# Optimization experiments

Hardware: AMD Instinct MI355X
Metric: run time of the kernel (lower is better)

## Reference

```python
import jax, jax.numpy as jnp
import numpy as np
from jax.scipy.special import logsumexp

UNK_ID = 1
B, T, V = 128, 33, 25000
E, H, D = 256, 256, 512
N, C = 8192, 16384
L = T - 1


def setup_inputs() -> dict:
    key = jax.random.key(0)
    ks = jax.random.split(key, 12)
    input_memories = jax.random.normal(ks[0], (N, D), jnp.float32)
    # each target owns a contiguous block of N//B memories (every segment non-empty)
    origin = jnp.repeat(jnp.arange(B, dtype=jnp.int32), N // B)
    initial_states = jax.random.normal(ks[1], (B, H), jnp.float32)
    target_token_ids = jax.random.randint(ks[2], (B, T), 0, V)
    # copyable elements: pick (memory n, time l); flat idx into [N,L] and [B,L]
    mem_pick = jax.random.randint(ks[3], (C,), 0, N)
    t_pick = jax.random.randint(ks[4], (C,), 0, L)
    copyable_elements_idxs = mem_pick * L + t_pick
    copyable_elements_sample_idxs = origin[mem_pick] * L + t_pick
    target_lengths = jax.random.randint(ks[5], (B,), 1, L + 1)
    emb_weight = 0.02 * jax.random.normal(ks[6], (V, E), jnp.float32)
    gru_w_ih = 0.05 * jax.random.normal(ks[7], (3 * H, E), jnp.float32)
    gru_w_hh = 0.05 * jax.random.normal(ks[8], (3 * H, H), jnp.float32)
    gru_b_ih = jnp.zeros((3 * H,), jnp.float32)
    gru_b_hh = jnp.zeros((3 * H,), jnp.float32)
    w_std_att = 0.05 * jax.random.normal(ks[9], (H, D), jnp.float32)
    w_copy_att = 0.05 * jax.random.normal(ks[10], (H, D), jnp.float32)
    hidden_to_vocab = 0.01 * jax.random.normal(ks[11], (2 * H, E), jnp.float32)
    vocab_bias = jnp.zeros((V,), jnp.float32)
    return dict(input_memories=input_memories, input_memories_origin_idx=origin,
                initial_states=initial_states, target_token_ids=target_token_ids,
                copyable_elements_idxs=copyable_elements_idxs,
                copyable_elements_sample_idxs=copyable_elements_sample_idxs,
                target_lengths=target_lengths, emb_weight=emb_weight,
                gru_w_ih=gru_w_ih, gru_w_hh=gru_w_hh, gru_b_ih=gru_b_ih,
                gru_b_hh=gru_b_hh, w_std_att=w_std_att, w_copy_att=w_copy_att,
                hidden_to_vocab=hidden_to_vocab, vocab_bias=vocab_bias)


def _gru(x, h0, w_ih, w_hh, b_ih, b_hh):
    # x: [B,L,E], h0: [B,H] -> outputs [B,L,H], last state [B,H]
    def step(h, xt):
        gi = xt @ w_ih.T + b_ih
        gh = h @ w_hh.T + b_hh
        ir, iz, inew = jnp.split(gi, 3, axis=-1)
        hr, hz, hnew = jnp.split(gh, 3, axis=-1)
        r = jax.nn.sigmoid(ir + hr)
        z = jax.nn.sigmoid(iz + hz)
        n = jnp.tanh(inew + r * hnew)
        h_next = (1.0 - z) * n + z * h
        return h_next, h_next
    h_last, ys = jax.lax.scan(step, h0, jnp.swapaxes(x, 0, 1))
    return jnp.swapaxes(ys, 0, 1), h_last


def _seg_log_softmax(x, idx, num_seg):
    m = jax.ops.segment_max(x, idx, num_segments=num_seg)
    x_sh = x - m[idx]
    s = jax.ops.segment_sum(jnp.exp(x_sh), idx, num_segments=num_seg)
    return x_sh - jnp.log(s)[idx]


def _seg_logsumexp(x, idx, num_seg):
    m = jax.ops.segment_max(x, idx, num_segments=num_seg)
    m_safe = jnp.where(jnp.isfinite(m), m, 0.0)
    s = jax.ops.segment_sum(jnp.exp(x - m_safe[idx]), idx, num_segments=num_seg)
    return jnp.where(s > 0, jnp.log(jnp.where(s > 0, s, 1.0)) + m_safe, -jnp.inf)


def reference(input_memories, input_memories_origin_idx, initial_states,
              target_token_ids, copyable_elements_idxs,
              copyable_elements_sample_idxs, target_lengths, emb_weight,
              gru_w_ih, gru_w_hh, gru_b_ih, gru_b_hh, w_std_att, w_copy_att,
              hidden_to_vocab, vocab_bias):
    origin = input_memories_origin_idx
    b, t = target_token_ids.shape
    l = t - 1
    tok_in = target_token_ids[:, :-1]
    tok_out = target_token_ids[:, 1:]

    x = emb_weight[tok_in]                                   # [B,L,E]
    out_states, _ = _gru(x, initial_states, gru_w_ih, gru_w_hh, gru_b_ih, gru_b_hh)
    std_reps = input_memories @ w_std_att.T                  # [N,H]
    copy_reps = input_memories @ w_copy_att.T                # [N,H]
    out_per_input = out_states[origin]                       # [N,L,H]
    std_scores = jnp.einsum('nlh,nh->nl', out_per_input, std_reps)
    copy_scores = jnp.einsum('nlh,nh->nl', out_per_input, copy_reps)

    std_logprobs = _seg_log_softmax(std_scores, origin, b)   # [N,L]
    std_mul = jnp.exp(std_logprobs)[:, :, None] * std_reps[:, None, :]
    std_out = jax.ops.segment_sum(std_mul, origin, num_segments=b)  # [B,L,H]

    cat = jnp.concatenate([std_out, out_states], axis=-1)    # [B,L,2H]
    target_scores = (cat @ hidden_to_vocab) @ emb_weight.T + vocab_bias  # [B,L,V]

    total_copy = _seg_logsumexp(copy_scores, origin, b)      # [B,L]
    all_scores = jnp.concatenate([target_scores, total_copy[:, :, None]], axis=-1)
    norm = logsumexp(all_scores, axis=-1)                    # [B,L]
    target_logprobs = target_scores - norm[:, :, None]
    copy_logprobs = copy_scores - norm[origin]               # [N,L]

    num_valid = jax.ops.segment_sum(jnp.ones_like(copyable_elements_sample_idxs),
                                    copyable_elements_sample_idxs,
                                    num_segments=b * l)
    valid_copy = num_valid.reshape(b, l) > 0
    unk_loc = tok_out == UNK_ID
    mask = valid_copy & unk_loc

    gen_lp = jnp.take_along_axis(target_logprobs, tok_out[:, :, None], axis=-1)[..., 0]
    gen_lp = jnp.where(mask, -jnp.inf, gen_lp)

    cc = _seg_logsumexp(copy_logprobs.reshape(-1)[copyable_elements_idxs],
                        copyable_elements_sample_idxs, b * l).reshape(b, l)

    any_lp = logsumexp(jnp.stack([gen_lp, cc]), axis=0)      # [B,L]
    len_mask = (jnp.arange(l)[None, :] < target_lengths[:, None]).astype(jnp.float32)
    per_seq = (any_lp * len_mask).sum(-1) / len_mask.sum(-1)
    return -per_seq.mean()
```

## Files before the change

### kernel.cpp

```cpp
#include <hip/hip_runtime.h>
#include <hip/hip_bf16.h>

#define UNK 1
constexpr int B  = 128, T = 33, V = 25000, E = 256, H = 256, D = 512;
constexpr int N  = 8192, C = 16384, L = 32;
constexpr int BL = B * L;
constexpr int VP = 25088;

typedef __attribute__((ext_vector_type(8))) short bf16x8;
typedef __attribute__((ext_vector_type(4))) float fx4;
typedef unsigned short u16;
typedef unsigned int u32;

__device__ __forceinline__ u16 f2b(float f) {
  u32 u = __float_as_uint(f);
  u += 0x7FFFu + ((u >> 16) & 1u);
  return (u16)(u >> 16);
}
__device__ __forceinline__ float b2f(u16 s) { return __uint_as_float(((u32)s) << 16); }
__device__ __forceinline__ float fsigm(float x) { return 1.f / (1.f + __expf(-x)); }
__device__ __forceinline__ float ftanh(float x) {
  float cx = fminf(fmaxf(x, -15.f), 15.f);
  float e = __expf(2.f * cx);
  return (e - 1.f) / (e + 1.f);
}
__device__ __forceinline__ u32 fkey(float f) {
  u32 b = __float_as_uint(f);
  return (b & 0x80000000u) ? ~b : (b | 0x80000000u);
}
__device__ __forceinline__ float fdec(u32 k) {
  u32 b = (k & 0x80000000u) ? (k & 0x7FFFFFFFu) : ~k;
  return __uint_as_float(b);
}
__device__ __forceinline__ void lcomb(float& M, float& S, float m2, float s2) {
  float Mn = fmaxf(M, m2);
  float a = (S  > 0.f) ? S  * expf(M  - Mn) : 0.f;
  float b = (s2 > 0.f) ? s2 * expf(m2 - Mn) : 0.f;
  M = Mn; S = a + b;
}
__device__ __forceinline__ void gload16(const void* g, void* l) {
  __builtin_amdgcn_global_load_lds(
      (const __attribute__((address_space(1))) void*)g,
      (__attribute__((address_space(3))) void*)l, 16, 0, 0);
}

__device__ __forceinline__ void cvt4_at(const float* in, u16* out, int i) {
  float4 v = *(const float4*)&in[i];
  u16 r[4] = { f2b(v.x), f2b(v.y), f2b(v.z), f2b(v.w) };
  *(ushort4*)&out[i] = *(ushort4*)r;
}

constexpr int EB_GI   = 192;
constexpr int P2_EMB  = VP * E / 1024;
constexpr int P2_MEM  = N * D / 1024;
constexpr int P2_WHH  = 192;
constexpr int P2_WS   = 128;
constexpr int P2_WC   = 128;
constexpr int P2_TR   = 512;
constexpr int P2_INIT = 16;
constexpr int EB2_TOT = EB_GI + P2_EMB + P2_MEM + P2_WHH + P2_WS + P2_WC + P2_TR + P2_INIT;

__global__ __launch_bounds__(256, 2) void k_embgiB2(const int* __restrict__ tok,
    const float* __restrict__ emb, const float* __restrict__ wih,
    const float* __restrict__ bih, const float* __restrict__ bhh,
    float* __restrict__ Git,
    const float* __restrict__ mem, const float* __restrict__ whh,
    const float* __restrict__ wstd, const float* __restrict__ wcpy,
    const float* __restrict__ h2v,
    u16* __restrict__ embb, u16* __restrict__ memb, u16* __restrict__ whb,
    u16* __restrict__ wsb, u16* __restrict__ wcb, u16* __restrict__ h2vtb,
    u32* __restrict__ segk, float* __restrict__ segs,
    int* __restrict__ nval, float* __restrict__ lacc) {
  __shared__ __align__(16) u16 As[2][128 * 64];
  __shared__ __align__(16) u16 Bs2[2][128 * 64];
  int e = blockIdx.x, t = threadIdx.x;
  if (e >= EB_GI) {
    int b = e - EB_GI;
    if (b < P2_EMB) {
      int i = (b * 256 + t) * 4;
      if (i + 3 < V * E) cvt4_at(emb, embb, i);
      else for (int j = 0; j < 4; ++j) embb[i + j] = (i + j < V * E) ? f2b(emb[i + j]) : (u16)0;
      return;
    }
    b -= P2_EMB;
    if (b < P2_MEM) { cvt4_at(mem, memb, (b * 256 + t) * 4); return; }
    b -= P2_MEM;
    if (b < P2_WHH) { cvt4_at(whh, whb, (b * 256 + t) * 4); return; }
    b -= P2_WHH;
    if (b < P2_WS)  { cvt4_at(wstd, wsb, (b * 256 + t) * 4); return; }
    b -= P2_WS;
    if (b < P2_WC)  { cvt4_at(wcpy, wcb, (b * 256 + t) * 4); return; }
    b -= P2_WC;
    if (b < P2_TR) {
      int f = b * 256 + t, j = f >> 9, k = f & 511;
      h2vtb[f] = f2b(h2v[k * 256 + j]);
      return;
    }
    b -= P2_TR;
    int i = b * 256 + t;
    if (i < BL) { segk[i] = 0x007FFFFFu; segs[i] = 0.f; nval[i] = 0; }
    if (i == 0) lacc[0] = 0.f;
    return;
  }
  int m0 = (e & 31) * 128, n0 = (e >> 5) * 128;
  int lane = t & 63, w = t >> 6, wm = w >> 1, wn = w & 1;
  int r16 = lane & 15, hi = lane >> 4;
  char* AsB = (char*)&As[0][0];
  char* BsB = (char*)&Bs2[0][0];
  int tk4[4];
#pragma unroll
  for (int i = 0; i < 4; ++i) {
    int row = (w * 4 + i) * 8 + (lane >> 3);
    int bl = m0 + row;
    tk4[i] = tok[(bl >> 5) * 33 + (bl & 31)];
  }
  fx4 acc[4][4] = {};
  auto stage = [&](int kt, int buf) {
#pragma unroll
    for (int i = 0; i < 4; ++i) {
      int row = (w * 4 + i) * 8 + (lane >> 3);
      int c = (lane & 7) ^ (row & 7);
      float4 a0 = *(const float4*)&emb[tk4[i] * 256 + kt * 64 + c * 8];
      float4 a1 = *(const float4*)&emb[tk4[i] * 256 + kt * 64 + c * 8 + 4];
      __align__(16) u16 ra[8] = { f2b(a0.x), f2b(a0.y), f2b(a0.z), f2b(a0.w),
                                  f2b(a1.x), f2b(a1.y), f2b(a1.z), f2b(a1.w) };
      *(int4*)(AsB + buf * 16384 + (w * 4 + i) * 1024 + lane * 16) = *(const int4*)ra;
      float4 b0 = *(const float4*)&wih[(n0 + row) * 256 + kt * 64 + c * 8];
      float4 b1 = *(const float4*)&wih[(n0 + row) * 256 + kt * 64 + c * 8 + 4];
      __align__(16) u16 rb[8] = { f2b(b0.x), f2b(b0.y), f2b(b0.z), f2b(b0.w),
                                  f2b(b1.x), f2b(b1.y), f2b(b1.z), f2b(b1.w) };
      *(int4*)(BsB + buf * 16384 + (w * 4 + i) * 1024 + lane * 16) = *(const int4*)rb;
    }
  };
  stage(0, 0);
  __syncthreads();
  for (int kt = 0; kt < 4; ++kt) {
    int buf = kt & 1;
    bf16x8 afr[4][2], bfr[4][2];
#pragma unroll
    for (int mi = 0; mi < 4; ++mi)
#pragma unroll
      for (int kk = 0; kk < 2; ++kk) {
        int row = wm * 64 + mi * 16 + r16, cc = kk * 4 + hi;
        afr[mi][kk] = *(const bf16x8*)(AsB + buf * 16384 + (row * 8 + (cc ^ (row & 7))) * 16);
      }
#pragma unroll
    for (int ni = 0; ni < 4; ++ni)
#pragma unroll
      for (int kk = 0; kk < 2; ++kk) {
        int row = wn * 64 + ni * 16 + r16, cc = kk * 4 + hi;
        bfr[ni][kk] = *(const bf16x8*)(BsB + buf * 16384 + (row * 8 + (cc ^ (row & 7))) * 16);
      }
    if (kt < 3) {
      stage(kt + 1, (kt + 1) & 1);
    }
#pragma unroll
    for (int kk = 0; kk < 2; ++kk)
#pragma unroll
      for (int mi = 0; mi < 4; ++mi)
#pragma unroll
        for (int ni = 0; ni < 4; ++ni)
          acc[mi][ni] = __builtin_amdgcn_mfma_f32_16x16x32_bf16(afr[mi][kk], bfr[ni][kk], acc[mi][ni], 0, 0, 0);
    __syncthreads();
  }
  float bihv[4];
#pragma unroll
  for (int ni = 0; ni < 4; ++ni) {
    int j = n0 + wn * 64 + ni * 16 + r16;
    bihv[ni] = bih[j] + (j < 512 ? bhh[j] : 0.f);
  }
#pragma unroll
  for (int mi = 0; mi < 4; ++mi)
#pragma unroll
    for (int ni = 0; ni < 4; ++ni)
#pragma unroll
      for (int q = 0; q < 4; ++q) {
        int bl = m0 + wm * 64 + mi * 16 + hi * 4 + q;
        int b = bl >> 5, st = bl & 31;
        int j  = n0 + wn * 64 + ni * 16 + r16;
        Git[(((size_t)(b >> 4) * 32 + st) * 768 + j) * 16 + (b & 15)] = acc[mi][ni][q] + bihv[ni];
      }
}

__global__ __launch_bounds__(512, 2) void k_grureps(
    const float* __restrict__ Git, const u16* __restrict__ whb,
    const float* __restrict__ bhh, const float* __restrict__ h0,
    u16* __restrict__ outsb,
    const u16* __restrict__ Am, const u16* __restrict__ wsb,
    const u16* __restrict__ wcb, float* __restrict__ sr, float* __restrict__ cr) {
  __shared__ __align__(16) char smem[147456];
  const int t = threadIdx.x;
  const int w = t >> 6, l = t & 63;

  if (blockIdx.x < 8) {
    u16* nfr = (u16*)smem;
    u16* hbf0 = (u16*)(smem + 131072);
    u16* hbf1 = (u16*)(smem + 131072 + 8192);
    const int lj = l & 15, lk = l >> 4;
    const int b0 = blockIdx.x * 16;

    bf16x8 fr[2][8], fz[2][8];
#pragma unroll
    for (int jh = 0; jh < 2; ++jh)
#pragma unroll
      for (int kc = 0; kc < 8; ++kc) {
        int jr = w * 32 + jh * 16 + lj;
        int k0 = kc * 32 + lk * 8;
        fr[jh][kc] = *(const bf16x8*)&whb[(0 * 256 + jr) * 256 + k0];
        fz[jh][kc] = *(const bf16x8*)&whb[(1 * 256 + jr) * 256 + k0];
        int4 nv = *(const int4*)&whb[(2 * 256 + jr) * 256 + k0];
        *(int4*)&nfr[((w * 16 + jh * 8 + kc) * 64 + l) * 8] = nv;
      }
    float bN[2];
#pragma unroll
    for (int jh = 0; jh < 2; ++jh) bN[jh] = bhh[512 + w * 32 + jh * 16 + lj];
    float hst[2][4];
#pragma unroll
    for (int jh = 0; jh < 2; ++jh)
#pragma unroll
      for (int q = 0; q < 4; ++q) {
        int m = lk * 4 + q, j = w * 32 + jh * 16 + lj;
        hst[jh][q] = h0[(b0 + m) * 256 + j];
        hbf0[m * 256 + (((j >> 3) ^ (m & 7)) * 8) + (j & 7)] = f2b(hst[jh][q]);
      }
    __syncthreads();

    for (int st = 0; st < 32; ++st) {
      const float* gb = Git + (size_t)(blockIdx.x * 32 + st) * 768 * 16;
      fx4 grz[4];
#pragma unroll
      for (int g = 0; g < 2; ++g)
#pragma unroll
        for (int jh = 0; jh < 2; ++jh)
          grz[g * 2 + jh] = *(const fx4*)&gb[(g * 256 + w * 32 + jh * 16 + lj) * 16 + lk * 4];
      fx4 gn[2];
      fx4 accR[2] = {}, accZ[2] = {}, accN[2] = {};
      const u16* hb = (st & 1) ? hbf1 : hbf0;
#pragma unroll
      for (int kc = 0; kc < 8; ++kc) {
        int k8 = kc * 4 + lk;
        bf16x8 a = *(const bf16x8*)&hb[lj * 256 + ((k8 ^ (lj & 7)) * 8)];
        bf16x8 nf0 = *(const bf16x8*)&nfr[((w * 16 + 0 + kc) * 64 + l) * 8];
        bf16x8 nf1 = *(const bf16x8*)&nfr[((w * 16 + 8 + kc) * 64 + l) * 8];
        accR[0] = __builtin_amdgcn_mfma_f32_16x16x32_bf16(a, fr[0][kc], accR[0], 0, 0, 0);
        accR[1] = __builtin_amdgcn_mfma_f32_16x16x32_bf16(a, fr[1][kc], accR[1], 0, 0, 0);
        accZ[0] = __builtin_amdgcn_mfma_f32_16x16x32_bf16(a, fz[0][kc], accZ[0], 0, 0, 0);
        accZ[1] = __builtin_amdgcn_mfma_f32_16x16x32_bf16(a, fz[1][kc], accZ[1], 0, 0, 0);
        accN[0] = __builtin_amdgcn_mfma_f32_16x16x32_bf16(a, nf0, accN[0], 0, 0, 0);
        accN[1] = __builtin_amdgcn_mfma_f32_16x16x32_bf16(a, nf1, accN[1], 0, 0, 0);
        if (kc == 5) {
#pragma unroll
          for (int jh = 0; jh < 2; ++jh)
            gn[jh] = *(const fx4*)&gb[(2 * 256 + w * 32 + jh * 16 + lj) * 16 + lk * 4];
        }
      }
      u16* hw = (st & 1) ? hbf0 : hbf1;
#pragma unroll
      for (int jh = 0; jh < 2; ++jh)
#pragma unroll
        for (int q = 0; q < 4; ++q) {
          float r = fsigm(grz[jh][q] + accR[jh][q]);
          float z = fsigm(grz[2 + jh][q] + accZ[jh][q]);
          float n = ftanh(gn[jh][q] + r * (accN[jh][q] + bN[jh]));
          float hn = (1.f - z) * n + z * hst[jh][q];
          hst[jh][q] = hn;
          int m = lk * 4 + q, j = w * 32 + jh * 16 + lj;
          u16 hbv = f2b(hn);
          hw[m * 256 + (((j >> 3) ^ (m & 7)) * 8) + (j & 7)] = hbv;
          outsb[((size_t)(b0 + m) * 32 + st) * 256 + j] = hbv;
        }
      __syncthreads();
    }
    return;
  }

  int rb = blockIdx.x - 8;
  int m0 = (rb >> 1) * 128, sn = rb & 1;
  const u16* Bsrc = sn ? wcb : wsb;
  int grp = w >> 2, wg = w & 3, wm = wg >> 1, wn = wg & 1;
  int jb = grp * 128;
  int lane = l, r16 = lane & 15, hi = lane >> 4;
  char* AsB = smem;
  char* BsB = smem + 32768 + grp * 32768;
  fx4 acc[4][4] = {};
  auto stage = [&](int kt, int buf) {
    if (grp == 0) {
#pragma unroll
      for (int i = 0; i < 4; ++i) {
        int s = (wg * 4 + i) * 64 + lane;
        int row = s >> 3, sw = s & 7, c = sw ^ (row & 7);
        gload16(&Am[(m0 + row) * 512 + kt * 64 + c * 8], AsB + buf * 16384 + (wg * 4 + i) * 1024);
        gload16(&Bsrc[(0 + row) * 512 + kt * 64 + c * 8], (smem + 32768) + buf * 16384 + (wg * 4 + i) * 1024);
      }
    } else {
#pragma unroll
      for (int i = 0; i < 4; ++i) {
        int s = (wg * 4 + i) * 64 + lane;
        int row = s >> 3, sw = s & 7, c = sw ^ (row & 7);
        gload16(&Bsrc[(128 + row) * 512 + kt * 64 + c * 8], (smem + 65536) + buf * 16384 + (wg * 4 + i) * 1024);
      }
    }
  };
  stage(0, 0);
  for (int kt = 0; kt < 8; ++kt) {
    __syncthreads();
    if (kt < 7) stage(kt + 1, (kt + 1) & 1);
    int buf = kt & 1;
    bf16x8 afr[4][2], bfr[4][2];
#pragma unroll
    for (int mi = 0; mi < 4; ++mi)
#pragma unroll
      for (int kk = 0; kk < 2; ++kk) {
        int row = wm * 64 + mi * 16 + r16, cc = kk * 4 + hi;
        afr[mi][kk] = *(const bf16x8*)(AsB + buf * 16384 + (row * 8 + (cc ^ (row & 7))) * 16);
      }
#pragma unroll
    for (int ni = 0; ni < 4; ++ni)
#pragma unroll
      for (int kk = 0; kk < 2; ++kk) {
        int row = wn * 64 + ni * 16 + r16, cc = kk * 4 + hi;
        bfr[ni][kk] = *(const bf16x8*)(BsB + buf * 16384 + (row * 8 + (cc ^ (row & 7))) * 16);
      }
#pragma unroll
    for (int kk = 0; kk < 2; ++kk)
#pragma unroll
      for (int mi = 0; mi < 4; ++mi)
#pragma unroll
        for (int ni = 0; ni < 4; ++ni)
          acc[mi][ni] = __builtin_amdgcn_mfma_f32_16x16x32_bf16(afr[mi][kk], bfr[ni][kk], acc[mi][ni], 0, 0, 0);
  }
#pragma unroll
  for (int mi = 0; mi < 4; ++mi)
#pragma unroll
    for (int ni = 0; ni < 4; ++ni)
#pragma unroll
      for (int q = 0; q < 4; ++q) {
        int mr = m0 + wm * 64 + mi * 16 + hi * 4 + q;
        int j  = sn * 256 + jb + wn * 64 + ni * 16 + r16;
        float vv = acc[mi][ni][q];
        if (j < 256) sr[mr * 256 + j] = vv; else cr[mr * 256 + (j - 256)] = vv;
      }
}

__global__ void k_scores(const u16* __restrict__ outsb, const float* __restrict__ sr,
                         const float* __restrict__ cr, float* __restrict__ ss,
                         float* __restrict__ cs) {
  __shared__ float os[32][257];
  int b = blockIdx.x >> 2, nc = blockIdx.x & 3, t = threadIdx.x;
  for (int i = 0; i < 8; ++i) {
    int q = t + 256 * i, row = q >> 6, c4 = q & 63;
    ushort4 v = *(const ushort4*)&outsb[(b * 32 + row) * 256 + c4 * 4];
    os[row][c4 * 4] = b2f(v.x); os[row][c4 * 4 + 1] = b2f(v.y);
    os[row][c4 * 4 + 2] = b2f(v.z); os[row][c4 * 4 + 3] = b2f(v.w);
  }
  __syncthreads();
  int l = t & 31, g = t >> 5;
  for (int rep = 0; rep < 2; ++rep) {
    int n = b * 64 + nc * 16 + g + rep * 8;
    float a = 0.f, c = 0.f;
    for (int k4 = 0; k4 < 64; ++k4) {
      float4 s4 = *(const float4*)&sr[n * 256 + k4 * 4];
      float4 c4v = *(const float4*)&cr[n * 256 + k4 * 4];
      float o0 = os[l][k4 * 4], o1 = os[l][k4 * 4 + 1];
      float o2 = os[l][k4 * 4 + 2], o3 = os[l][k4 * 4 + 3];
      a = fmaf(o0, s4.x, a); a = fmaf(o1, s4.y, a);
      a = fmaf(o2, s4.z, a); a = fmaf(o3, s4.w, a);
      c = fmaf(o0, c4v.x, c); c = fmaf(o1, c4v.y, c);
      c = fmaf(o2, c4v.z, c); c = fmaf(o3, c4v.w, c);
    }
    ss[n * 32 + l] = a; cs[n * 32 + l] = c;
  }
}

__global__ void k_smxseg(const float* __restrict__ ss, const float* __restrict__ cs,
                         const float* __restrict__ sr, u16* __restrict__ sob,
                         float* __restrict__ tc,
                         const int* __restrict__ idx, const int* __restrict__ sid,
                         u32* __restrict__ sk, int* __restrict__ nv) {
  __shared__ float wst[64][33];
  __shared__ float wcp[64][33];
  int e = blockIdx.x, t = threadIdx.x;
  if (e >= 128) {
    int c = (e - 128) * 256 + t;
    if (c < C) {
      int s = sid[c];
      atomicMax(&sk[s], fkey(cs[idx[c]]));
      atomicAdd(&nv[s], 1);
    }
    return;
  }
  int b = e;
  for (int i = 0; i < 8; ++i) {
    int q = t + 256 * i;
    wst[q >> 5][q & 31] = ss[b * 2048 + q];
    wcp[q >> 5][q & 31] = cs[b * 2048 + q];
  }
  __syncthreads();
  if (t < 32) {
    int l = t; float m = -1e30f;
    for (int n = 0; n < 64; ++n) m = fmaxf(m, wst[n][l]);
    float s = 0.f;
    for (int n = 0; n < 64; ++n) s += expf(wst[n][l] - m);
    float inv = 1.f / s;
    for (int n = 0; n < 64; ++n) wst[n][l] = expf(wst[n][l] - m) * inv;
  } else if (t < 64) {
    int l = t - 32; float m = -1e30f;
    for (int n = 0; n < 64; ++n) m = fmaxf(m, wcp[n][l]);
    float s = 0.f;
    for (int n = 0; n < 64; ++n) s += expf(wcp[n][l] - m);
    tc[b * 32 + l] = m + logf(s);
  }
  __syncthreads();
  float acc[32] = {};
  for (int n = 0; n < 64; ++n) {
    float v = sr[(b * 64 + n) * 256 + t];
#pragma unroll
    for (int l = 0; l < 32; ++l) acc[l] = fmaf(wst[n][l], v, acc[l]);
  }
  for (int l = 0; l < 32; ++l) sob[(b * 32 + l) * 256 + t] = f2b(acc[l]);
}

__global__ __launch_bounds__(256, 2) void k_projseg(const u16* __restrict__ sob,
    const u16* __restrict__ outsb, const u16* __restrict__ h2vtb,
    u16* __restrict__ pb,
    const int* __restrict__ idx, const int* __restrict__ sid,
    const float* __restrict__ cs, const u32* __restrict__ sk,
    float* __restrict__ ssum) {
  __shared__ __align__(16) u16 As[2][128 * 64];
  __shared__ __align__(16) u16 Bs2[2][128 * 64];
  int e = blockIdx.x, t = threadIdx.x;
  if (e >= 64) {
    int c = (e - 64) * 256 + t;
    if (c < C) {
      int s = sid[c];
      atomicAdd(&ssum[s], __expf(cs[idx[c]] - fdec(sk[s])));
    }
    return;
  }
  int m0 = (e & 31) * 128, n0 = (e >> 5) * 128;
  int lane = t & 63, w = t >> 6, wm = w >> 1, wn = w & 1;
  int r16 = lane & 15, hi = lane >> 4;
  char* AsB = (char*)&As[0][0];
  char* BsB = (char*)&Bs2[0][0];
  fx4 acc[4][4] = {};
  auto stage = [&](int kt, int buf) {
    const u16* Asrc = (kt < 4) ? sob : outsb;
    int ko = (kt & 3) * 64;
#pragma unroll
    for (int i = 0; i < 4; ++i) {
      int s = (w * 4 + i) * 64 + lane;
      int row = s >> 3, sw = s & 7, c = sw ^ (row & 7);
      gload16(&Asrc[(m0 + row) * 256 + ko + c * 8], AsB + buf * 16384 + (w * 4 + i) * 1024);
      gload16(&h2vtb[(n0 + row) * 512 + kt * 64 + c * 8], BsB + buf * 16384 + (w * 4 + i) * 1024);
    }
  };
  stage(0, 0);
  for (int kt = 0; kt < 8; ++kt) {
    __syncthreads();
    if (kt < 7) stage(kt + 1, (kt + 1) & 1);
    int buf = kt & 1;
    bf16x8 afr[4][2], bfr[4][2];
#pragma unroll
    for (int mi = 0; mi < 4; ++mi)
#pragma unroll
      for (int kk = 0; kk < 2; ++kk) {
        int row = wm * 64 + mi * 16 + r16, cc = kk * 4 + hi;
        afr[mi][kk] = *(const bf16x8*)(AsB + buf * 16384 + (row * 8 + (cc ^ (row & 7))) * 16);
      }
#pragma unroll
    for (int ni = 0; ni < 4; ++ni)
#pragma unroll
      for (int kk = 0; kk < 2; ++kk) {
        int row = wn * 64 + ni * 16 + r16, cc = kk * 4 + hi;
        bfr[ni][kk] = *(const bf16x8*)(BsB + buf * 16384 + (row * 8 + (cc ^ (row & 7))) * 16);
      }
#pragma unroll
    for (int kk = 0; kk < 2; ++kk)
#pragma unroll
      for (int mi = 0; mi < 4; ++mi)
#pragma unroll
        for (int ni = 0; ni < 4; ++ni)
          acc[mi][ni] = __builtin_amdgcn_mfma_f32_16x16x32_bf16(afr[mi][kk], bfr[ni][kk], acc[mi][ni], 0, 0, 0);
  }
#pragma unroll
  for (int mi = 0; mi < 4; ++mi)
#pragma unroll
    for (int ni = 0; ni < 4; ++ni)
#pragma unroll
      for (int q = 0; q < 4; ++q) {
        int mr = m0 + wm * 64 + mi * 16 + hi * 4 + q;
        int j  = n0 + wn * 64 + ni * 16 + r16;
        pb[mr * 256 + j] = f2b(acc[mi][ni][q]);
      }
}

__global__ __launch_bounds__(256, 2) void k_gemmgen(const u16* __restrict__ A,
    const u16* __restrict__ Bm, const float* __restrict__ vb,
    float* __restrict__ parts,
    const int* __restrict__ tok, float* __restrict__ gs) {
  __shared__ __align__(16) u16 Bs[2][64 * 256];
  __shared__ float red[2][128];
  int e = blockIdx.x, t = threadIdx.x;
  if (e >= 256) {
    int w = t >> 6, lane = t & 63;
    int row = (e - 256) * 4 + w;
    int b = row >> 5, l = row & 31;
    int tk = tok[b * 33 + l + 1];
    float s = 0.f;
#pragma unroll
    for (int i = 0; i < 4; ++i) {
      int k = lane * 4 + i;
      s += b2f(A[row * 256 + k]) * b2f(Bm[tk * 256 + k]);
    }
#pragma unroll
    for (int d = 1; d < 64; d <<= 1) s += __shfl_xor(s, d);
    if (lane == 0) gs[row] = s + vb[tk];
    return;
  }
  int vr = e & 7, mch = e >> 3;
  int m0 = mch * 128;
  int c0 = vr * 49, cn = 49;
  int lane = t & 63, w = t >> 6, wm = w >> 1, wn = w & 1;
  int r16 = lane & 15, hi = lane >> 4;
  char* BsB = (char*)&Bs[0][0];
  const char* Bb = (const char*)Bm;

  bf16x8 af[4][8];
#pragma unroll
  for (int mi = 0; mi < 4; ++mi)
#pragma unroll
    for (int ks = 0; ks < 8; ++ks)
      af[mi][ks] = *(const bf16x8*)&A[(m0 + wm * 64 + mi * 16 + r16) * 256 + ks * 32 + hi * 8];

  int soff[8];
#pragma unroll
  for (int i = 0; i < 8; ++i) {
    int s = (w * 8 + i) * 64 + lane;
    int row = s >> 5, c = s & 31;
    int gc = (c & ~7) | ((c & 7) ^ (row & 7));
    soff[i] = row * 512 + gc * 16;
  }

  float Sa[4][4] = {};

#define STAGE(CG, BUF)                                                        \
  {                                                                           \
    _Pragma("unroll")                                                         \
    for (int i = 0; i < 8; ++i)                                               \
      gload16(Bb + (CG) * 32768 + soff[i],                                    \
              BsB + (BUF) * 32768 + w * 8192 + i * 1024);                     \
  }

  STAGE(c0, 0);
  for (int c = 0; c < cn; ++c) {
    int cg = c0 + c;
    __syncthreads();
    if (c + 1 < cn) STAGE(cg + 1, (c + 1) & 1);
    int buf = c & 1;
    fx4 acc[4][2] = {};
#pragma unroll
    for (int ks = 0; ks < 8; ++ks)
#pragma unroll
      for (int ni = 0; ni < 2; ++ni) {
        int row = wn * 32 + ni * 16 + r16;
        int g = ks * 4 + hi;
        int gp = (g & ~7) | ((g & 7) ^ (row & 7));
        bf16x8 bfv = *(const bf16x8*)(BsB + buf * 32768 + row * 512 + gp * 16);
#pragma unroll
        for (int mi = 0; mi < 4; ++mi)
          acc[mi][ni] = __builtin_amdgcn_mfma_f32_16x16x32_bf16(af[mi][ks], bfv, acc[mi][ni], 0, 0, 0);
      }
    float bias[2];
#pragma unroll
    for (int ni = 0; ni < 2; ++ni) {
      int v = cg * 64 + wn * 32 + ni * 16 + r16;
      bias[ni] = (v < V) ? vb[v] : -1e30f;
    }
#pragma unroll
    for (int mi = 0; mi < 4; ++mi)
#pragma unroll
      for (int q = 0; q < 4; ++q) {
        float ev = __expf(acc[mi][0][q] + bias[0]) + __expf(acc[mi][1][q] + bias[1]);
        Sa[mi][q] += ev;
      }
  }
#undef STAGE

#pragma unroll
  for (int mi = 0; mi < 4; ++mi)
#pragma unroll
    for (int q = 0; q < 4; ++q) {
      float s = Sa[mi][q];
#pragma unroll
      for (int d = 1; d < 16; d <<= 1) s += __shfl_xor(s, d);
      Sa[mi][q] = s;
    }
  if (r16 == 0) {
#pragma unroll
    for (int mi = 0; mi < 4; ++mi)
#pragma unroll
      for (int q = 0; q < 4; ++q)
        red[wn][wm * 64 + mi * 16 + hi * 4 + q] = Sa[mi][q];
  }
  __syncthreads();
  if (t < 128)
    parts[(m0 + t) * 8 + vr] = red[0][t] + red[1][t];
}

__global__ void k_final(const float* __restrict__ parts, const float* __restrict__ tc,
                        const float* __restrict__ gs, const u32* __restrict__ sk,
                        const float* __restrict__ ssum, const int* __restrict__ nv,
                        const int* __restrict__ tok, const int* __restrict__ tlen,
                        float* __restrict__ lacc) {
  int i = blockIdx.x * 256 + threadIdx.x;
  int b = i >> 5, l = i & 31;
  float S = 0.f;
#pragma unroll
  for (int r = 0; r < 8; ++r) S += parts[i * 8 + r];
  float M = 0.f, Ss = S;
  lcomb(M, Ss, tc[i], 1.f);
  float nrm = M + logf(Ss);
  int tk = tok[b * 33 + l + 1];
  float glp = gs[i] - nrm;
  int cnt = nv[i];
  if (cnt > 0 && tk == UNK) glp = -INFINITY;
  float cc = (cnt > 0) ? (logf(ssum[i]) + fdec(sk[i]) - nrm) : -INFINITY;
  float m = fmaxf(glp, cc);
  float any = (m == -INFINITY) ? -INFINITY : m + logf(expf(glp - m) + expf(cc - m));
  float oa = (l < tlen[b]) ? any : 0.f;
#pragma unroll
  for (int d = 1; d < 32; d <<= 1) oa += __shfl_xor(oa, d);
  if (l == 0) atomicAdd(lacc, oa / (float)tlen[b]);
}

__global__ void k_loss(const float* __restrict__ lacc, float* __restrict__ out) {
  out[0] = -lacc[0] / 128.f;
}

extern "C" void kernel_launch(void* const* d_in, const int* in_sizes, int n_in,
                              void* d_out, int out_size, void* d_ws, size_t ws_size,
                              hipStream_t stream) {
  const float* mem  = (const float*)d_in[0];
  const float* h0   = (const float*)d_in[2];
  const int*   tok  = (const int*)d_in[3];
  const int*   cidx = (const int*)d_in[4];
  const int*   csid = (const int*)d_in[5];
  const int*   tlen = (const int*)d_in[6];
  const float* emb  = (const float*)d_in[7];
  const float* wih  = (const float*)d_in[8];
  const float* whh  = (const float*)d_in[9];
  const float* bih  = (const float*)d_in[10];
  const float* bhh  = (const float*)d_in[11];
  const float* wstd = (const float*)d_in[12];
  const float* wcpy = (const float*)d_in[13];
  const float* h2v  = (const float*)d_in[14];
  const float* vb   = (const float*)d_in[15];

  char* ws = (char*)d_ws;
  size_t off = 0;
  auto alloc = [&](size_t bytes) -> char* {
    char* p = ws + off;
    off = (off + bytes + 255) & ~(size_t)255;
    return p;
  };
  u16*    embb  = (u16*)   alloc((size_t)VP * E * 2);
  u16*    memb  = (u16*)   alloc((size_t)N * D * 2);
  u16*    whb   = (u16*)   alloc(768 * 256 * 2);
  u16*    wsb   = (u16*)   alloc(256 * 512 * 2);
  u16*    wcb   = (u16*)   alloc(256 * 512 * 2);
  u16*    h2vtb = (u16*)   alloc(256 * 512 * 2);
  float*  Git   = (float*) alloc((size_t)BL * 768 * 4);
  u16*    outsb = (u16*)   alloc((size_t)BL * 256 * 2);
  u16*    stdob = (u16*)   alloc((size_t)BL * 256 * 2);
  float*  sreps = (float*) alloc((size_t)N * 256 * 4);
  float*  creps = (float*) alloc((size_t)N * 256 * 4);
  float*  sscr  = (float*) alloc((size_t)N * 32 * 4);
  float*  cscr  = (float*) alloc((size_t)N * 32 * 4);
  float*  tcopy = (float*) alloc(BL * 4);
  u16*    projb = (u16*)   alloc((size_t)BL * 256 * 2);
  float*  parts = (float*) alloc((size_t)BL * 8 * 4);
  float*  gens  = (float*) alloc(BL * 4);
  u32*    segk  = (u32*)   alloc(BL * 4);
  float*  segs  = (float*) alloc(BL * 4);
  int*    nval  = (int*)   alloc(BL * 4);
  float*  lacc  = (float*) alloc(256);
  (void)ws_size; (void)in_sizes; (void)n_in; (void)out_size;

  k_embgiB2<<<EB2_TOT, 256, 0, stream>>>(tok, emb, wih, bih, bhh, Git,
                                         mem, whh, wstd, wcpy, h2v,
                                         embb, memb, whb, wsb, wcb, h2vtb,
                                         segk, segs, nval, lacc);
  k_grureps<<<136, 512, 0, stream>>>(Git, whb, bhh, h0, outsb,
                                     memb, wsb, wcb, sreps, creps);
  k_scores<<<512, 256, 0, stream>>>(outsb, sreps, creps, sscr, cscr);
  k_smxseg<<<192, 256, 0, stream>>>(sscr, cscr, sreps, stdob, tcopy,
                                    cidx, csid, segk, nval);
  k_projseg<<<128, 256, 0, stream>>>(stdob, outsb, h2vtb, projb,
                                     cidx, csid, cscr, segk, segs);
  k_gemmgen<<<1280, 256, 0, stream>>>(projb, embb, vb, parts, tok, gens);
  k_final<<<16, 256, 0, stream>>>(parts, tcopy, gens, segk, segs, nval, tok, tlen, lacc);
  k_loss<<<1, 1, 0, stream>>>(lacc, (float*)d_out);
}
```

Measured before the change: 283.4 us.

## Move embedding conversion into GRU kernel and split vocab GEMM sixteen ways

```diff
diff --git a/kernel.cpp b/kernel.cpp
--- a/kernel.cpp
+++ b/kernel.cpp
@@ -51,14 +51,11 @@
 }
 
 constexpr int EB_GI   = 192;
-constexpr int P2_EMB  = VP * E / 1024;
 constexpr int P2_MEM  = N * D / 1024;
 constexpr int P2_WHH  = 192;
 constexpr int P2_WS   = 128;
 constexpr int P2_WC   = 128;
-constexpr int P2_TR   = 512;
-constexpr int P2_INIT = 16;
-constexpr int EB2_TOT = EB_GI + P2_EMB + P2_MEM + P2_WHH + P2_WS + P2_WC + P2_TR + P2_INIT;
+constexpr int EB2_TOT = EB_GI + P2_MEM + P2_WHH + P2_WS + P2_WC;
 
 __global__ __launch_bounds__(256, 2) void k_embgiB2(const int* __restrict__ tok,
     const float* __restrict__ emb, const float* __restrict__ wih,
@@ -66,40 +63,20 @@
     float* __restrict__ Git,
     const float* __restrict__ mem, const float* __restrict__ whh,
     const float* __restrict__ wstd, const float* __restrict__ wcpy,
-    const float* __restrict__ h2v,
-    u16* __restrict__ embb, u16* __restrict__ memb, u16* __restrict__ whb,
-    u16* __restrict__ wsb, u16* __restrict__ wcb, u16* __restrict__ h2vtb,
-    u32* __restrict__ segk, float* __restrict__ segs,
-    int* __restrict__ nval, float* __restrict__ lacc) {
+    u16* __restrict__ memb, u16* __restrict__ whb,
+    u16* __restrict__ wsb, u16* __restrict__ wcb) {
   __shared__ __align__(16) u16 As[2][128 * 64];
   __shared__ __align__(16) u16 Bs2[2][128 * 64];
   int e = blockIdx.x, t = threadIdx.x;
   if (e >= EB_GI) {
     int b = e - EB_GI;
-    if (b < P2_EMB) {
-      int i = (b * 256 + t) * 4;
-      if (i + 3 < V * E) cvt4_at(emb, embb, i);
-      else for (int j = 0; j < 4; ++j) embb[i + j] = (i + j < V * E) ? f2b(emb[i + j]) : (u16)0;
-      return;
-    }
-    b -= P2_EMB;
     if (b < P2_MEM) { cvt4_at(mem, memb, (b * 256 + t) * 4); return; }
     b -= P2_MEM;
     if (b < P2_WHH) { cvt4_at(whh, whb, (b * 256 + t) * 4); return; }
     b -= P2_WHH;
     if (b < P2_WS)  { cvt4_at(wstd, wsb, (b * 256 + t) * 4); return; }
     b -= P2_WS;
-    if (b < P2_WC)  { cvt4_at(wcpy, wcb, (b * 256 + t) * 4); return; }
-    b -= P2_WC;
-    if (b < P2_TR) {
-      int f = b * 256 + t, j = f >> 9, k = f & 511;
-      h2vtb[f] = f2b(h2v[k * 256 + j]);
-      return;
-    }
-    b -= P2_TR;
-    int i = b * 256 + t;
-    if (i < BL) { segk[i] = 0x007FFFFFu; segs[i] = 0.f; nval[i] = 0; }
-    if (i == 0) lacc[0] = 0.f;
+    cvt4_at(wcpy, wcb, (b * 256 + t) * 4);
     return;
   }
   int m0 = (e & 31) * 128, n0 = (e >> 5) * 128;
@@ -182,17 +159,49 @@
       }
 }
 
+constexpr int GR_GRU  = 8;
+constexpr int GR_REPS = 128;
+constexpr int GR_EMB  = VP * E / 2048;
+constexpr int GR_TR   = 256;
+constexpr int GR_INIT = 8;
+constexpr int GR_TOT  = GR_GRU + GR_REPS + GR_EMB + GR_TR + GR_INIT;
+
 __global__ __launch_bounds__(512, 2) void k_grureps(
     const float* __restrict__ Git, const u16* __restrict__ whb,
     const float* __restrict__ bhh, const float* __restrict__ h0,
     u16* __restrict__ outsb,
     const u16* __restrict__ Am, const u16* __restrict__ wsb,
-    const u16* __restrict__ wcb, float* __restrict__ sr, float* __restrict__ cr) {
+    const u16* __restrict__ wcb, float* __restrict__ sr, float* __restrict__ cr,
+    const float* __restrict__ emb, const float* __restrict__ h2v,
+    u16* __restrict__ embb, u16* __restrict__ h2vtb,
+    u32* __restrict__ segk, float* __restrict__ segs,
+    int* __restrict__ nval, float* __restrict__ lacc) {
   __shared__ __align__(16) char smem[147456];
   const int t = threadIdx.x;
   const int w = t >> 6, l = t & 63;
 
-  if (blockIdx.x < 8) {
+  if (blockIdx.x >= GR_GRU + GR_REPS) {
+    int b = blockIdx.x - (GR_GRU + GR_REPS);
+    if (b < GR_EMB) {
+      int i = (b * 512 + t) * 4;
+      if (i + 3 < V * E) cvt4_at(emb, embb, i);
+      else for (int j = 0; j < 4; ++j) embb[i + j] = (i + j < V * E) ? f2b(emb[i + j]) : (u16)0;
+      return;
+    }
+    b -= GR_EMB;
+    if (b < GR_TR) {
+      int f = b * 512 + t, j = f >> 9, k = f & 511;
+      h2vtb[f] = f2b(h2v[k * 256 + j]);
+      return;
+    }
+    b -= GR_TR;
+    int i = b * 512 + t;
+    if (i < BL) { segk[i] = 0x007FFFFFu; segs[i] = 0.f; nval[i] = 0; }
+    if (i == 0) lacc[0] = 0.f;
+    return;
+  }
+
+  if (blockIdx.x < GR_GRU) {
     u16* nfr = (u16*)smem;
     u16* hbf0 = (u16*)(smem + 131072);
     u16* hbf1 = (u16*)(smem + 131072 + 8192);
@@ -274,7 +283,7 @@
     return;
   }
 
-  int rb = blockIdx.x - 8;
+  int rb = blockIdx.x - GR_GRU;
   int m0 = (rb >> 1) * 128, sn = rb & 1;
   const u16* Bsrc = sn ? wcb : wsb;
   int grp = w >> 2, wg = w & 3, wm = wg >> 1, wn = wg & 1;
@@ -501,9 +510,9 @@
   __shared__ __align__(16) u16 Bs[2][64 * 256];
   __shared__ float red[2][128];
   int e = blockIdx.x, t = threadIdx.x;
-  if (e >= 256) {
+  if (e >= 512) {
     int w = t >> 6, lane = t & 63;
-    int row = (e - 256) * 4 + w;
+    int row = (e - 512) * 4 + w;
     int b = row >> 5, l = row & 31;
     int tk = tok[b * 33 + l + 1];
     float s = 0.f;
@@ -517,9 +526,10 @@
     if (lane == 0) gs[row] = s + vb[tk];
     return;
   }
-  int vr = e & 7, mch = e >> 3;
+  int vr = e & 15, mch = e >> 4;
   int m0 = mch * 128;
-  int c0 = vr * 49, cn = 49;
+  int c0 = vr * 24 + min(vr, 8);
+  int cn = 24 + (vr < 8 ? 1 : 0);
   int lane = t & 63, w = t >> 6, wm = w >> 1, wn = w & 1;
   int r16 = lane & 15, hi = lane >> 4;
   char* BsB = (char*)&Bs[0][0];
@@ -604,7 +614,7 @@
   }
   __syncthreads();
   if (t < 128)
-    parts[(m0 + t) * 8 + vr] = red[0][t] + red[1][t];
+    parts[(size_t)(m0 + t) * 16 + vr] = red[0][t] + red[1][t];
 }
 
 __global__ void k_final(const float* __restrict__ parts, const float* __restrict__ tc,
@@ -616,7 +626,7 @@
   int b = i >> 5, l = i & 31;
   float S = 0.f;
 #pragma unroll
-  for (int r = 0; r < 8; ++r) S += parts[i * 8 + r];
+  for (int r = 0; r < 16; ++r) S += parts[(size_t)i * 16 + r];
   float M = 0.f, Ss = S;
   lcomb(M, Ss, tc[i], 1.f);
   float nrm = M + logf(Ss);
@@ -678,7 +688,7 @@
   float*  cscr  = (float*) alloc((size_t)N * 32 * 4);
   float*  tcopy = (float*) alloc(BL * 4);
   u16*    projb = (u16*)   alloc((size_t)BL * 256 * 2);
-  float*  parts = (float*) alloc((size_t)BL * 8 * 4);
+  float*  parts = (float*) alloc((size_t)BL * 16 * 4);
   float*  gens  = (float*) alloc(BL * 4);
   u32*    segk  = (u32*)   alloc(BL * 4);
   float*  segs  = (float*) alloc(BL * 4);
@@ -687,17 +697,18 @@
   (void)ws_size; (void)in_sizes; (void)n_in; (void)out_size;
 
   k_embgiB2<<<EB2_TOT, 256, 0, stream>>>(tok, emb, wih, bih, bhh, Git,
-                                         mem, whh, wstd, wcpy, h2v,
-                                         embb, memb, whb, wsb, wcb, h2vtb,
-                                         segk, segs, nval, lacc);
-  k_grureps<<<136, 512, 0, stream>>>(Git, whb, bhh, h0, outsb,
-                                     memb, wsb, wcb, sreps, creps);
+                                         mem, whh, wstd, wcpy,
+                                         memb, whb, wsb, wcb);
+  k_grureps<<<GR_TOT, 512, 0, stream>>>(Git, whb, bhh, h0, outsb,
+                                        memb, wsb, wcb, sreps, creps,
+                                        emb, h2v, embb, h2vtb,
+                                        segk, segs, nval, lacc);
   k_scores<<<512, 256, 0, stream>>>(outsb, sreps, creps, sscr, cscr);
   k_smxseg<<<192, 256, 0, stream>>>(sscr, cscr, sreps, stdob, tcopy,
                                     cidx, csid, segk, nval);
   k_projseg<<<128, 256, 0, stream>>>(stdob, outsb, h2vtb, projb,
                                      cidx, csid, cscr, segk, segs);
-  k_gemmgen<<<1280, 256, 0, stream>>>(projb, embb, vb, parts, tok, gens);
+  k_gemmgen<<<1536, 256, 0, stream>>>(projb, embb, vb, parts, tok, gens);
   k_final<<<16, 256, 0, stream>>>(parts, tcopy, gens, segk, segs, nval, tok, tlen, lacc);
   k_loss<<<1, 1, 0, stream>>>(lacc, (float*)d_out);
 }
```

Result: faster. 247.5 us (-12.7%).
